# Kernel tuning notes

Measured on AMD Instinct MI355X. Metric: run time of the kernel, lower is better.

Reference implementation:

```python
import jax, jax.numpy as jnp
import numpy as np

N, E = 32, 512          # graphs per batch, padded nodes per graph
IN_DIM = 128            # in_dim
OUT_DIM = 64            # out_dim (d)
N_TYPE = 3              # config.num_edge_type
Q_DIM = 128             # config.input_dim (q_update=False)


def setup_inputs() -> dict:
    key = jax.random.key(0)
    ks = jax.random.split(key, 8)
    s = 0.05  # weight init scale (stands in for xavier_uniform)
    return {
        "input_state": jax.random.normal(ks[0], (N, E, IN_DIM), jnp.float32),
        "adj": jax.random.randint(ks[1], (N, E, E), 0, N_TYPE + 1, jnp.int32),
        "query_vec": jax.random.normal(ks[2], (N, Q_DIM), jnp.float32),
        "node_mask": jax.random.uniform(ks[3], (N, E, 1), jnp.float32),
        "W_type": jax.random.normal(ks[4], (N_TYPE, IN_DIM, OUT_DIM), jnp.float32) * s,
        "a_type": jax.random.normal(ks[5], (N_TYPE, 2 * OUT_DIM, 1), jnp.float32) * s,
        "qattn_W1": jax.random.normal(ks[6], (N_TYPE, Q_DIM, 2 * OUT_DIM), jnp.float32) * s,
        "qattn_W2": jax.random.normal(ks[7], (N_TYPE, 2 * OUT_DIM, 2 * OUT_DIM), jnp.float32) * s,
    }


def reference(input_state, adj, query_vec, node_mask, W_type, a_type, qattn_W1, qattn_W2):
    # Per-type node projections: (T, N, E, d). Dropout omitted (eval mode, p=0).
    h_all = jnp.einsum("nei,tio->tneo", input_state, W_type)

    # Query gate per type: sigmoid(relu(q @ W1) @ W2) -> (T, N, 2d)
    qg = jax.nn.relu(jnp.einsum("nq,tqc->tnc", query_vec, qattn_W1))
    qg = jax.nn.sigmoid(jnp.einsum("tnc,tcd->tnd", qg, qattn_W2))

    d = h_all.shape[-1]
    a_src = a_type[:, :d, 0]   # (T, d) applied to the repeated (source) half
    a_dst = a_type[:, d:, 0]   # (T, d) applied to the tiled (target) half

    # score[t,n,i,j] = lrelu( (h[t,n,i]*qg1[t,n]) . a_src[t] + (h[t,n,j]*qg2[t,n]) . a_dst[t] )
    # This is exactly cat([h_i, h_j]) * q_gate @ a without materializing (N,E,E,2d).
    s_src = jnp.einsum("tned,tnd,td->tne", h_all, qg[..., :d], a_src)
    s_dst = jnp.einsum("tned,tnd,td->tne", h_all, qg[..., d:], a_dst)
    score = jax.nn.leaky_relu(s_src[:, :, :, None] + s_dst[:, :, None, :], 0.2)  # (T,N,E,E)

    # Accumulate scores where adj matches each edge type (1-indexed).
    type_ids = jnp.arange(1, N_TYPE + 1, dtype=adj.dtype)[:, None, None, None]
    scores = jnp.sum(jnp.where(adj[None] == type_ids, score, 0.0), axis=0)  # (N,E,E)

    # Mask non-edges and softmax over dim=2 (target nodes).
    scores = jnp.where(adj > 0, scores, jnp.float32(-1e30))
    coefs = jax.nn.softmax(scores, axis=2)

    # h from the last edge-type loop iteration, node-masked.
    h = h_all[-1] * node_mask  # (N,E,d)

    # out[n,j,:] = sum_i coefs[n,i,j] * h[n,i,:]  (sum over dim=1 in the torch code)
    return jnp.einsum("nij,nid->njd", coefs, h)
```

## Files before the change

kernel.cpp:

```cpp
#include <hip/hip_runtime.h>
#include <hip/hip_bf16.h>

#define N_G 32
#define E_N 512
#define IN_D 128
#define OUT_D 64
#define NT 3
#define Q_D 128

#define WS_WSRC 0
#define WS_WDST 12288
#define WS_SSRC 24576
#define WS_SDST 73728
#define WS_RINV 139264
#define WS_H    155648
#define WS_W2T  679936
#define WS_ADJ2 684032

typedef const float* fp;
typedef __attribute__((ext_vector_type(8))) short short8x;
typedef __attribute__((ext_vector_type(4))) float float4x;

static __device__ inline ushort f2bf(float x) {
  __hip_bfloat16 b = __float2bfloat16(x);
  return *(ushort*)&b;
}
static __device__ inline float bf2f(ushort u) {
  return __uint_as_float((uint)u << 16);
}

__global__ __launch_bounds__(256) void k1_qgate_pack(
    fp qv_g, fp Wt, fp at, fp W1, fp W2,
    const int* __restrict__ adj, float* __restrict__ ws) {
  const int b = blockIdx.x;
  const int t = threadIdx.x;

  if (b >= 96) {
    const int w = t >> 6, lane = t & 63;
    const int R = (b - 96) * 4 + w;
    const int* arow = adj + (size_t)R * E_N;
    uint pack = 0;
    #pragma unroll
    for (int bb = 0; bb < 8; bb++) {
      int a = arow[bb * 64 + lane];
      pack |= (uint)(a & 3) << (2 * bb);
    }
    ((ushort*)(ws + WS_ADJ2))[(size_t)R * 64 + lane] = (ushort)pack;
    return;
  }

  const int tb = b >> 5;
  const int n  = b & 31;
  __shared__ float qv[128];
  __shared__ float ps[8][132];
  __shared__ float g1s[128], g2s[128];
  __shared__ float gsv[64], gdv[64];
  const int h   = t >> 5;
  const int cg_ = (t & 31) << 2;

  if (t < 128) qv[t] = qv_g[n * Q_D + t];
  __syncthreads();

  {
    float a0 = 0.f, a1 = 0.f, a2 = 0.f, a3 = 0.f;
    const float* Wp = W1 + tb * 16384 + (h * 16) * 128 + cg_;
    #pragma unroll
    for (int q = 0; q < 16; q++) {
      float4 wv4 = *(const float4*)(Wp + q * 128);
      float qq = qv[h * 16 + q];
      a0 += qq * wv4.x; a1 += qq * wv4.y; a2 += qq * wv4.z; a3 += qq * wv4.w;
    }
    ps[h][cg_ + 0] = a0; ps[h][cg_ + 1] = a1;
    ps[h][cg_ + 2] = a2; ps[h][cg_ + 3] = a3;
  }
  __syncthreads();
  if (t < 128) {
    float s = 0.f;
    #pragma unroll
    for (int k = 0; k < 8; k++) s += ps[k][t];
    g1s[t] = s > 0.f ? s : 0.f;
  }
  __syncthreads();

  {
    float a0 = 0.f, a1 = 0.f, a2 = 0.f, a3 = 0.f;
    const float* Wp = W2 + tb * 16384 + (h * 16) * 128 + cg_;
    #pragma unroll
    for (int q = 0; q < 16; q++) {
      float4 wv4 = *(const float4*)(Wp + q * 128);
      float qq = g1s[h * 16 + q];
      a0 += qq * wv4.x; a1 += qq * wv4.y; a2 += qq * wv4.z; a3 += qq * wv4.w;
    }
    ps[h][cg_ + 0] = a0; ps[h][cg_ + 1] = a1;
    ps[h][cg_ + 2] = a2; ps[h][cg_ + 3] = a3;
  }
  __syncthreads();
  if (t < 128) {
    float s = 0.f;
    #pragma unroll
    for (int k = 0; k < 8; k++) s += ps[k][t];
    g2s[t] = 1.f / (1.f + __expf(-s));
  }
  __syncthreads();
  if (t < 64) {
    gsv[t] = g2s[t] * at[tb * 128 + t];
    gdv[t] = g2s[64 + t] * at[tb * 128 + 64 + t];
  }
  __syncthreads();

  {
    const int i = t & 127, hf = t >> 7;
    float as = 0.f, ad = 0.f;
    const float* Wp = Wt + tb * 8192 + i * 64 + hf * 32;
    #pragma unroll
    for (int dj = 0; dj < 8; dj++) {
      float4 wv4 = *(const float4*)(Wp + dj * 4);
      const float* gp = gsv + hf * 32 + dj * 4;
      const float* gq = gdv + hf * 32 + dj * 4;
      as += wv4.x * gp[0] + wv4.y * gp[1] + wv4.z * gp[2] + wv4.w * gp[3];
      ad += wv4.x * gq[0] + wv4.y * gq[1] + wv4.z * gq[2] + wv4.w * gq[3];
    }
    ps[hf][i]     = as;
    ps[2 + hf][i] = ad;
  }
  __syncthreads();
  if (t < 128) {
    ws[WS_WSRC + tb * 4096 + n * 128 + t] = ps[0][t] + ps[1][t];
    ws[WS_WDST + tb * 4096 + n * 128 + t] = ps[2][t] + ps[3][t];
  }
  if (tb == 2 && t < 128) {
    int f = n * 256 + t * 2;
    int d = f >> 7, i0 = f & 127;
    uint lo = f2bf(Wt[2 * 8192 + i0 * 64 + d]);
    uint hi = f2bf(Wt[2 * 8192 + (i0 + 1) * 64 + d]);
    ((uint*)(ws + WS_W2T))[f >> 1] = lo | (hi << 16);
  }
}

__global__ __launch_bounds__(256) void k2_h_s(fp X, fp mask,
                                              float* __restrict__ ws) {
  const int n  = blockIdx.x & 31;
  const int e0 = (blockIdx.x >> 5) << 5;
  __shared__ ushort A[32 * 136];
  __shared__ ushort BT[64 * 136];
  __shared__ ushort eT[64 * 40];
  __shared__ float wv[6 * 128];
  const int t = threadIdx.x;
  ushort* hb = (ushort*)(ws + WS_H);
  const ushort* w2t = (const ushort*)(ws + WS_W2T);

  #pragma unroll
  for (int k = 0; k < 4; k++) {
    int f = t + 256 * k;
    int e = f >> 5, iq = f & 31;
    float4 v = *(const float4*)&X[(n * E_N + e0 + e) * IN_D + iq * 4];
    uint2 pk;
    pk.x = (uint)f2bf(v.x) | ((uint)f2bf(v.y) << 16);
    pk.y = (uint)f2bf(v.z) | ((uint)f2bf(v.w) << 16);
    *(uint2*)&A[e * 136 + iq * 4] = pk;
  }
  #pragma unroll
  for (int k = 0; k < 4; k++) {
    int f = t + 256 * k;
    int d = f >> 4, iq8 = f & 15;
    *(uint4*)&BT[d * 136 + iq8 * 8] = *(const uint4*)&w2t[d * 128 + iq8 * 8];
  }
  #pragma unroll
  for (int k = 0; k < 3; k++) {
    int idx = t + 256 * k;
    int row = idx >> 7, i = idx & 127;
    wv[idx] = (row < 3) ? ws[WS_WSRC + row * 4096 + n * 128 + i]
                        : ws[WS_WDST + (row - 3) * 4096 + n * 128 + i];
  }
  __syncthreads();

  const int w = t >> 6, lane = t & 63;
  const int m15 = lane & 15, quad = lane >> 4;
  const int msub = w & 1, dhalf = w >> 1;

  float4x acc2[2];
  acc2[0] = (float4x)(0.f); acc2[1] = (float4x)(0.f);
  #pragma unroll
  for (int ks = 0; ks < 4; ks++) {
    short8x af = *(const short8x*)&A[(msub * 16 + m15) * 136 + ks * 32 + quad * 8];
    #pragma unroll
    for (int dd = 0; dd < 2; dd++) {
      short8x bfv = *(const short8x*)&BT[((dhalf * 2 + dd) * 16 + m15) * 136 + ks * 32 + quad * 8];
      acc2[dd] = __builtin_amdgcn_mfma_f32_16x16x32_bf16(af, bfv, acc2[dd], 0, 0, 0);
    }
  }

  if (t < 192) {
    const int e = t / 6, q = t % 6;
    float acc = 0.f;
    #pragma unroll
    for (int i8 = 0; i8 < 16; i8++) {
      uint4 pk = *(const uint4*)&A[e * 136 + i8 * 8];
      const float* wp = &wv[q * 128 + i8 * 8];
      acc += bf2f((ushort)(pk.x & 0xffff)) * wp[0];
      acc += bf2f((ushort)(pk.x >> 16))    * wp[1];
      acc += bf2f((ushort)(pk.y & 0xffff)) * wp[2];
      acc += bf2f((ushort)(pk.y >> 16))    * wp[3];
      acc += bf2f((ushort)(pk.z & 0xffff)) * wp[4];
      acc += bf2f((ushort)(pk.z >> 16))    * wp[5];
      acc += bf2f((ushort)(pk.w & 0xffff)) * wp[6];
      acc += bf2f((ushort)(pk.w >> 16))    * wp[7];
    }
    if (q < 3) ws[WS_SSRC + q * 16384 + n * 512 + e0 + e] = acc;
    else       ws[WS_SDST + (q - 3) * 16384 + n * 512 + e0 + e] = acc;
  }

  float mv[4];
  #pragma unroll
  for (int rg = 0; rg < 4; rg++)
    mv[rg] = mask[n * E_N + e0 + msub * 16 + quad * 4 + rg];
  #pragma unroll
  for (int dd = 0; dd < 2; dd++) {
    int dRow = (dhalf * 2 + dd) * 16 + m15;
    #pragma unroll
    for (int rg = 0; rg < 4; rg++) {
      int e = msub * 16 + quad * 4 + rg;
      eT[dRow * 40 + e] = f2bf(acc2[dd][rg] * mv[rg]);
    }
  }
  __syncthreads();

  {
    int d = t >> 2, e8 = t & 3;
    *(uint4*)&hb[(n * 64 + d) * 512 + e0 + e8 * 8] =
        *(const uint4*)&eT[d * 40 + e8 * 8];
  }
}

__global__ __launch_bounds__(256) void k3_rows(float* __restrict__ ws) {
  const int n  = blockIdx.x & 31;
  const int rb = (blockIdx.x >> 5) << 5;
  __shared__ float sd[3 * 512];
  const int t = threadIdx.x;
  const ushort* adj2 = (const ushort*)(ws + WS_ADJ2);

  #pragma unroll
  for (int k = 0; k < 6; k++) {
    int idx = t + 256 * k;
    sd[idx] = ws[WS_SDST + (idx >> 9) * 16384 + n * 512 + (idx & 511)];
  }
  __syncthreads();

  const int wave = t >> 6, lane = t & 63;
  #pragma unroll
  for (int rr = 0; rr < 8; rr++) {
    const int i = rb + wave * 8 + rr;
    const float s0 = ws[WS_SSRC + 0 * 16384 + n * 512 + i];
    const float s1 = ws[WS_SSRC + 1 * 16384 + n * 512 + i];
    const float s2 = ws[WS_SSRC + 2 * 16384 + n * 512 + i];
    uint pk = adj2[(size_t)(n * E_N + i) * 64 + lane];

    float sum = 0.f;
    #pragma unroll
    for (int bb = 0; bb < 8; bb++) {
      int a = (pk >> (2 * bb)) & 3;
      if (a > 0) {
        float s = (a == 1) ? s0 : (a == 2 ? s1 : s2);
        float v = s + sd[(a - 1) * 512 + bb * 64 + lane];
        v = v > 0.f ? v : 0.2f * v;
        sum += __expf(v);
      }
    }
    #pragma unroll
    for (int off = 32; off >= 1; off >>= 1) sum += __shfl_xor(sum, off, 64);
    if (lane == 0) ws[WS_RINV + n * 512 + i] = 1.f / sum;
  }
}

__global__ __launch_bounds__(256) void k4_out(float* __restrict__ ws,
                                              float* __restrict__ out) {
  const int n  = blockIdx.x & 31;
  const int j0 = (blockIdx.x >> 5) << 5;
  __shared__ ushort cT[32 * 136];
  __shared__ ushort hT[64 * 136];
  __shared__ ushort aS[128 * 64];
  __shared__ float sdT[3 * 32];
  __shared__ float ssT[3 * 128];
  __shared__ float riT[128];
  const int t = threadIdx.x;
  const ushort* hb = (const ushort*)(ws + WS_H);
  const ushort* adj2 = (const ushort*)(ws + WS_ADJ2);

  if (t < 96) sdT[t] = ws[WS_SDST + (t >> 5) * 16384 + n * 512 + j0 + (t & 31)];

  const int w = t >> 6, lane = t & 63;
  const int m15 = lane & 15, quad = lane >> 4;
  const int msub = w & 1, dhalf = w >> 1;
  const int c   = t & 31;
  const int rpb = t >> 5;
  const int u     = (j0 & 63) + c;
  const int shift = 2 * (j0 >> 6);

  float4x acc[2];
  acc[0] = (float4x)(0.f); acc[1] = (float4x)(0.f);

  for (int it = 0; it < 4; it++) {
    const int i0 = it << 7;

    #pragma unroll
    for (int k = 0; k < 4; k++) {
      int f = t + 256 * k;
      int d = f >> 4, i16 = f & 15;
      *(uint4*)&hT[d * 136 + i16 * 8] =
          *(const uint4*)&hb[(n * 64 + d) * 512 + i0 + i16 * 8];
    }
    #pragma unroll
    for (int k = 0; k < 4; k++) {
      int f = t + 256 * k;
      int r = f >> 3, c8 = f & 7;
      *(uint4*)&aS[r * 64 + c8 * 8] =
          *(const uint4*)&adj2[(size_t)(n * E_N + i0 + r) * 64 + c8 * 8];
    }
    #pragma unroll
    for (int k = 0; k < 2; k++) {
      int idx = t + 256 * k;
      if (idx < 128) riT[idx] = ws[WS_RINV + n * 512 + i0 + idx];
      else {
        int j2 = idx - 128;
        ssT[j2] = ws[WS_SSRC + (j2 >> 7) * 16384 + n * 512 + i0 + (j2 & 127)];
      }
    }
    __syncthreads();

    #pragma unroll
    for (int k = 0; k < 8; k++) {
      int r0 = 2 * (rpb + 8 * k);
      uint pack = 0;
      int a = (aS[r0 * 64 + u] >> shift) & 3;
      if (a > 0) {
        float v = ssT[(a - 1) * 128 + r0] + sdT[(a - 1) * 32 + c];
        v = v > 0.f ? v : 0.2f * v;
        pack = f2bf(__expf(v) * riT[r0]);
      }
      a = (aS[(r0 + 1) * 64 + u] >> shift) & 3;
      if (a > 0) {
        float v = ssT[(a - 1) * 128 + r0 + 1] + sdT[(a - 1) * 32 + c];
        v = v > 0.f ? v : 0.2f * v;
        pack |= (uint)f2bf(__expf(v) * riT[r0 + 1]) << 16;
      }
      *(uint*)&cT[c * 136 + r0] = pack;
    }
    __syncthreads();

    #pragma unroll
    for (int ks = 0; ks < 4; ks++) {
      short8x af = *(const short8x*)&cT[(msub * 16 + m15) * 136 + ks * 32 + quad * 8];
      #pragma unroll
      for (int dd = 0; dd < 2; dd++) {
        short8x bfv = *(const short8x*)&hT[((dhalf * 2 + dd) * 16 + m15) * 136 + ks * 32 + quad * 8];
        acc[dd] = __builtin_amdgcn_mfma_f32_16x16x32_bf16(af, bfv, acc[dd], 0, 0, 0);
      }
    }
    __syncthreads();
  }

  #pragma unroll
  for (int dd = 0; dd < 2; dd++)
    #pragma unroll
    for (int rg = 0; rg < 4; rg++) {
      int j = j0 + msub * 16 + quad * 4 + rg;
      out[(n * E_N + j) * 64 + (dhalf * 2 + dd) * 16 + m15] = acc[dd][rg];
    }
}

extern "C" void kernel_launch(void* const* d_in, const int* in_sizes, int n_in,
                              void* d_out, int out_size, void* d_ws, size_t ws_size,
                              hipStream_t stream) {
  fp input_state  = (fp)d_in[0];
  const int* adj  = (const int*)d_in[1];
  fp query_vec    = (fp)d_in[2];
  fp node_mask    = (fp)d_in[3];
  fp W_type       = (fp)d_in[4];
  fp a_type       = (fp)d_in[5];
  fp qattn_W1     = (fp)d_in[6];
  fp qattn_W2     = (fp)d_in[7];
  float* out = (float*)d_out;
  float* ws  = (float*)d_ws;

  k1_qgate_pack<<<96 + 4096, 256, 0, stream>>>(query_vec, W_type, a_type,
                                               qattn_W1, qattn_W2, adj, ws);
  k2_h_s<<<512, 256, 0, stream>>>(input_state, node_mask, ws);
  k3_rows<<<512, 256, 0, stream>>>(ws);
  k4_out<<<512, 256, 0, stream>>>(ws, out);
}
```

Before: 128.2 us.

## Fuse qgate into projection kernel and adj packing into row-stats kernel

The query-gate computation is merged into the projection/score kernel, so each block recomputes the gated attention vectors for its graph in shared memory instead of writing them to and reading them back from workspace. The adjacency 2-bit packing moves from the first kernel into the row-softmax-denominator kernel, which now reads raw adj once and both packs it and accumulates exp sums. This removes one launch and one full pass over adj. The cost is that each of the 256 blocks repeats the three-type qgate math, and there are half as many blocks for the projection work. Block indexing in the output kernel is also reordered so consecutive blocks share a graph.

```diff
diff --git a/kernel.cpp b/kernel.cpp
--- a/kernel.cpp
+++ b/kernel.cpp
@@ -8,13 +8,10 @@
 #define NT 3
 #define Q_D 128
 
-#define WS_WSRC 0
-#define WS_WDST 12288
 #define WS_SSRC 24576
 #define WS_SDST 73728
 #define WS_RINV 139264
 #define WS_H    155648
-#define WS_W2T  679936
 #define WS_ADJ2 684032
 
 typedef const float* fp;
@@ -29,215 +26,187 @@
   return __uint_as_float((uint)u << 16);
 }
 
-__global__ __launch_bounds__(256) void k1_qgate_pack(
-    fp qv_g, fp Wt, fp at, fp W1, fp W2,
-    const int* __restrict__ adj, float* __restrict__ ws) {
-  const int b = blockIdx.x;
-  const int t = threadIdx.x;
-
-  if (b >= 96) {
-    const int w = t >> 6, lane = t & 63;
-    const int R = (b - 96) * 4 + w;
-    const int* arow = adj + (size_t)R * E_N;
-    uint pack = 0;
-    #pragma unroll
-    for (int bb = 0; bb < 8; bb++) {
-      int a = arow[bb * 64 + lane];
-      pack |= (uint)(a & 3) << (2 * bb);
-    }
-    ((ushort*)(ws + WS_ADJ2))[(size_t)R * 64 + lane] = (ushort)pack;
-    return;
-  }
-
-  const int tb = b >> 5;
-  const int n  = b & 31;
+__global__ __launch_bounds__(256) void kA_qgate_h_s(
+    fp X, fp mask, fp qv_g, fp Wt, fp at, fp W1, fp W2,
+    float* __restrict__ ws) {
+  const int n  = blockIdx.x >> 3;
+  const int eh = blockIdx.x & 7;
   __shared__ float qv[128];
   __shared__ float ps[8][132];
   __shared__ float g1s[128], g2s[128];
   __shared__ float gsv[64], gdv[64];
+  __shared__ float wv[6 * 128];
+  __shared__ ushort BT[64 * 136];
+  __shared__ ushort A[32 * 136];
+  __shared__ ushort eT[64 * 40];
+  const int t = threadIdx.x;
+  ushort* hb = (ushort*)(ws + WS_H);
+
+  #pragma unroll
+  for (int k = 0; k < 8; k++) {
+    int f = k * 1024 + t * 4;
+    int i = f >> 6, d = f & 63;
+    float4 v = *(const float4*)&Wt[2 * 8192 + f];
+    BT[(d + 0) * 136 + i] = f2bf(v.x);
+    BT[(d + 1) * 136 + i] = f2bf(v.y);
+    BT[(d + 2) * 136 + i] = f2bf(v.z);
+    BT[(d + 3) * 136 + i] = f2bf(v.w);
+  }
+  if (t < 128) qv[t] = qv_g[n * Q_D + t];
+  __syncthreads();
+
   const int h   = t >> 5;
   const int cg_ = (t & 31) << 2;
-
-  if (t < 128) qv[t] = qv_g[n * Q_D + t];
-  __syncthreads();
-
-  {
-    float a0 = 0.f, a1 = 0.f, a2 = 0.f, a3 = 0.f;
-    const float* Wp = W1 + tb * 16384 + (h * 16) * 128 + cg_;
-    #pragma unroll
-    for (int q = 0; q < 16; q++) {
-      float4 wv4 = *(const float4*)(Wp + q * 128);
-      float qq = qv[h * 16 + q];
-      a0 += qq * wv4.x; a1 += qq * wv4.y; a2 += qq * wv4.z; a3 += qq * wv4.w;
-    }
-    ps[h][cg_ + 0] = a0; ps[h][cg_ + 1] = a1;
-    ps[h][cg_ + 2] = a2; ps[h][cg_ + 3] = a3;
-  }
-  __syncthreads();
-  if (t < 128) {
-    float s = 0.f;
-    #pragma unroll
-    for (int k = 0; k < 8; k++) s += ps[k][t];
-    g1s[t] = s > 0.f ? s : 0.f;
-  }
-  __syncthreads();
-
-  {
-    float a0 = 0.f, a1 = 0.f, a2 = 0.f, a3 = 0.f;
-    const float* Wp = W2 + tb * 16384 + (h * 16) * 128 + cg_;
-    #pragma unroll
-    for (int q = 0; q < 16; q++) {
-      float4 wv4 = *(const float4*)(Wp + q * 128);
-      float qq = g1s[h * 16 + q];
-      a0 += qq * wv4.x; a1 += qq * wv4.y; a2 += qq * wv4.z; a3 += qq * wv4.w;
-    }
-    ps[h][cg_ + 0] = a0; ps[h][cg_ + 1] = a1;
-    ps[h][cg_ + 2] = a2; ps[h][cg_ + 3] = a3;
-  }
-  __syncthreads();
-  if (t < 128) {
-    float s = 0.f;
-    #pragma unroll
-    for (int k = 0; k < 8; k++) s += ps[k][t];
-    g2s[t] = 1.f / (1.f + __expf(-s));
-  }
-  __syncthreads();
-  if (t < 64) {
-    gsv[t] = g2s[t] * at[tb * 128 + t];
-    gdv[t] = g2s[64 + t] * at[tb * 128 + 64 + t];
-  }
-  __syncthreads();
-
-  {
-    const int i = t & 127, hf = t >> 7;
-    float as = 0.f, ad = 0.f;
-    const float* Wp = Wt + tb * 8192 + i * 64 + hf * 32;
-    #pragma unroll
-    for (int dj = 0; dj < 8; dj++) {
-      float4 wv4 = *(const float4*)(Wp + dj * 4);
-      const float* gp = gsv + hf * 32 + dj * 4;
-      const float* gq = gdv + hf * 32 + dj * 4;
-      as += wv4.x * gp[0] + wv4.y * gp[1] + wv4.z * gp[2] + wv4.w * gp[3];
-      ad += wv4.x * gq[0] + wv4.y * gq[1] + wv4.z * gq[2] + wv4.w * gq[3];
-    }
-    ps[hf][i]     = as;
-    ps[2 + hf][i] = ad;
-  }
-  __syncthreads();
-  if (t < 128) {
-    ws[WS_WSRC + tb * 4096 + n * 128 + t] = ps[0][t] + ps[1][t];
-    ws[WS_WDST + tb * 4096 + n * 128 + t] = ps[2][t] + ps[3][t];
-  }
-  if (tb == 2 && t < 128) {
-    int f = n * 256 + t * 2;
-    int d = f >> 7, i0 = f & 127;
-    uint lo = f2bf(Wt[2 * 8192 + i0 * 64 + d]);
-    uint hi = f2bf(Wt[2 * 8192 + (i0 + 1) * 64 + d]);
-    ((uint*)(ws + WS_W2T))[f >> 1] = lo | (hi << 16);
-  }
-}
-
-__global__ __launch_bounds__(256) void k2_h_s(fp X, fp mask,
-                                              float* __restrict__ ws) {
-  const int n  = blockIdx.x & 31;
-  const int e0 = (blockIdx.x >> 5) << 5;
-  __shared__ ushort A[32 * 136];
-  __shared__ ushort BT[64 * 136];
-  __shared__ ushort eT[64 * 40];
-  __shared__ float wv[6 * 128];
-  const int t = threadIdx.x;
-  ushort* hb = (ushort*)(ws + WS_H);
-  const ushort* w2t = (const ushort*)(ws + WS_W2T);
-
-  #pragma unroll
-  for (int k = 0; k < 4; k++) {
-    int f = t + 256 * k;
-    int e = f >> 5, iq = f & 31;
-    float4 v = *(const float4*)&X[(n * E_N + e0 + e) * IN_D + iq * 4];
-    uint2 pk;
-    pk.x = (uint)f2bf(v.x) | ((uint)f2bf(v.y) << 16);
-    pk.y = (uint)f2bf(v.z) | ((uint)f2bf(v.w) << 16);
-    *(uint2*)&A[e * 136 + iq * 4] = pk;
-  }
-  #pragma unroll
-  for (int k = 0; k < 4; k++) {
-    int f = t + 256 * k;
-    int d = f >> 4, iq8 = f & 15;
-    *(uint4*)&BT[d * 136 + iq8 * 8] = *(const uint4*)&w2t[d * 128 + iq8 * 8];
-  }
-  #pragma unroll
-  for (int k = 0; k < 3; k++) {
-    int idx = t + 256 * k;
-    int row = idx >> 7, i = idx & 127;
-    wv[idx] = (row < 3) ? ws[WS_WSRC + row * 4096 + n * 128 + i]
-                        : ws[WS_WDST + (row - 3) * 4096 + n * 128 + i];
-  }
-  __syncthreads();
+  for (int tt = 0; tt < 3; tt++) {
+    {
+      float a0 = 0.f, a1 = 0.f, a2 = 0.f, a3 = 0.f;
+      const float* Wp = W1 + tt * 16384 + (h * 16) * 128 + cg_;
+      #pragma unroll
+      for (int q = 0; q < 16; q++) {
+        float4 wv4 = *(const float4*)(Wp + q * 128);
+        float qq = qv[h * 16 + q];
+        a0 += qq * wv4.x; a1 += qq * wv4.y; a2 += qq * wv4.z; a3 += qq * wv4.w;
+      }
+      ps[h][cg_ + 0] = a0; ps[h][cg_ + 1] = a1;
+      ps[h][cg_ + 2] = a2; ps[h][cg_ + 3] = a3;
+    }
+    __syncthreads();
+    if (t < 128) {
+      float s = 0.f;
+      #pragma unroll
+      for (int k = 0; k < 8; k++) s += ps[k][t];
+      g1s[t] = s > 0.f ? s : 0.f;
+    }
+    __syncthreads();
+    {
+      float a0 = 0.f, a1 = 0.f, a2 = 0.f, a3 = 0.f;
+      const float* Wp = W2 + tt * 16384 + (h * 16) * 128 + cg_;
+      #pragma unroll
+      for (int q = 0; q < 16; q++) {
+        float4 wv4 = *(const float4*)(Wp + q * 128);
+        float qq = g1s[h * 16 + q];
+        a0 += qq * wv4.x; a1 += qq * wv4.y; a2 += qq * wv4.z; a3 += qq * wv4.w;
+      }
+      ps[h][cg_ + 0] = a0; ps[h][cg_ + 1] = a1;
+      ps[h][cg_ + 2] = a2; ps[h][cg_ + 3] = a3;
+    }
+    __syncthreads();
+    if (t < 128) {
+      float s = 0.f;
+      #pragma unroll
+      for (int k = 0; k < 8; k++) s += ps[k][t];
+      g2s[t] = 1.f / (1.f + __expf(-s));
+    }
+    __syncthreads();
+    if (t < 64) {
+      gsv[t] = g2s[t] * at[tt * 128 + t];
+      gdv[t] = g2s[64 + t] * at[tt * 128 + 64 + t];
+    }
+    __syncthreads();
+    {
+      const int i = t & 127, hf = t >> 7;
+      float as = 0.f, ad = 0.f;
+      const float* Wp = Wt + tt * 8192 + i * 64 + hf * 32;
+      #pragma unroll
+      for (int dj = 0; dj < 8; dj++) {
+        float4 wv4 = *(const float4*)(Wp + dj * 4);
+        const float* gp = gsv + hf * 32 + dj * 4;
+        const float* gq = gdv + hf * 32 + dj * 4;
+        as += wv4.x * gp[0] + wv4.y * gp[1] + wv4.z * gp[2] + wv4.w * gp[3];
+        ad += wv4.x * gq[0] + wv4.y * gq[1] + wv4.z * gq[2] + wv4.w * gq[3];
+      }
+      ps[hf][i]     = as;
+      ps[2 + hf][i] = ad;
+    }
+    __syncthreads();
+    if (t < 128) {
+      wv[tt * 128 + t]       = ps[0][t] + ps[1][t];
+      wv[(3 + tt) * 128 + t] = ps[2][t] + ps[3][t];
+    }
+    __syncthreads();
+  }
 
   const int w = t >> 6, lane = t & 63;
   const int m15 = lane & 15, quad = lane >> 4;
   const int msub = w & 1, dhalf = w >> 1;
 
-  float4x acc2[2];
-  acc2[0] = (float4x)(0.f); acc2[1] = (float4x)(0.f);
-  #pragma unroll
-  for (int ks = 0; ks < 4; ks++) {
-    short8x af = *(const short8x*)&A[(msub * 16 + m15) * 136 + ks * 32 + quad * 8];
+  for (int sub = 0; sub < 2; sub++) {
+    const int e0 = eh * 64 + sub * 32;
+
+    #pragma unroll
+    for (int k = 0; k < 4; k++) {
+      int f = t + 256 * k;
+      int e = f >> 5, iq = f & 31;
+      float4 v = *(const float4*)&X[(n * E_N + e0 + e) * IN_D + iq * 4];
+      uint2 pk;
+      pk.x = (uint)f2bf(v.x) | ((uint)f2bf(v.y) << 16);
+      pk.y = (uint)f2bf(v.z) | ((uint)f2bf(v.w) << 16);
+      *(uint2*)&A[e * 136 + iq * 4] = pk;
+    }
+    __syncthreads();
+
+    float4x acc2[2];
+    acc2[0] = (float4x)(0.f); acc2[1] = (float4x)(0.f);
+    #pragma unroll
+    for (int ks = 0; ks < 4; ks++) {
+      short8x af = *(const short8x*)&A[(msub * 16 + m15) * 136 + ks * 32 + quad * 8];
+      #pragma unroll
+      for (int dd = 0; dd < 2; dd++) {
+        short8x bfv = *(const short8x*)&BT[((dhalf * 2 + dd) * 16 + m15) * 136 + ks * 32 + quad * 8];
+        acc2[dd] = __builtin_amdgcn_mfma_f32_16x16x32_bf16(af, bfv, acc2[dd], 0, 0, 0);
+      }
+    }
+
+    if (t < 192) {
+      const int e = t / 6, q = t % 6;
+      float acc = 0.f;
+      #pragma unroll
+      for (int i8 = 0; i8 < 16; i8++) {
+        uint4 pk = *(const uint4*)&A[e * 136 + i8 * 8];
+        const float* wp = &wv[q * 128 + i8 * 8];
+        acc += bf2f((ushort)(pk.x & 0xffff)) * wp[0];
+        acc += bf2f((ushort)(pk.x >> 16))    * wp[1];
+        acc += bf2f((ushort)(pk.y & 0xffff)) * wp[2];
+        acc += bf2f((ushort)(pk.y >> 16))    * wp[3];
+        acc += bf2f((ushort)(pk.z & 0xffff)) * wp[4];
+        acc += bf2f((ushort)(pk.z >> 16))    * wp[5];
+        acc += bf2f((ushort)(pk.w & 0xffff)) * wp[6];
+        acc += bf2f((ushort)(pk.w >> 16))    * wp[7];
+      }
+      if (q < 3) ws[WS_SSRC + q * 16384 + n * 512 + e0 + e] = acc;
+      else       ws[WS_SDST + (q - 3) * 16384 + n * 512 + e0 + e] = acc;
+    }
+
+    float mv[4];
+    #pragma unroll
+    for (int rg = 0; rg < 4; rg++)
+      mv[rg] = mask[n * E_N + e0 + msub * 16 + quad * 4 + rg];
     #pragma unroll
     for (int dd = 0; dd < 2; dd++) {
-      short8x bfv = *(const short8x*)&BT[((dhalf * 2 + dd) * 16 + m15) * 136 + ks * 32 + quad * 8];
-      acc2[dd] = __builtin_amdgcn_mfma_f32_16x16x32_bf16(af, bfv, acc2[dd], 0, 0, 0);
-    }
-  }
-
-  if (t < 192) {
-    const int e = t / 6, q = t % 6;
-    float acc = 0.f;
-    #pragma unroll
-    for (int i8 = 0; i8 < 16; i8++) {
-      uint4 pk = *(const uint4*)&A[e * 136 + i8 * 8];
-      const float* wp = &wv[q * 128 + i8 * 8];
-      acc += bf2f((ushort)(pk.x & 0xffff)) * wp[0];
-      acc += bf2f((ushort)(pk.x >> 16))    * wp[1];
-      acc += bf2f((ushort)(pk.y & 0xffff)) * wp[2];
-      acc += bf2f((ushort)(pk.y >> 16))    * wp[3];
-      acc += bf2f((ushort)(pk.z & 0xffff)) * wp[4];
-      acc += bf2f((ushort)(pk.z >> 16))    * wp[5];
-      acc += bf2f((ushort)(pk.w & 0xffff)) * wp[6];
-      acc += bf2f((ushort)(pk.w >> 16))    * wp[7];
-    }
-    if (q < 3) ws[WS_SSRC + q * 16384 + n * 512 + e0 + e] = acc;
-    else       ws[WS_SDST + (q - 3) * 16384 + n * 512 + e0 + e] = acc;
-  }
-
-  float mv[4];
-  #pragma unroll
-  for (int rg = 0; rg < 4; rg++)
-    mv[rg] = mask[n * E_N + e0 + msub * 16 + quad * 4 + rg];
-  #pragma unroll
-  for (int dd = 0; dd < 2; dd++) {
-    int dRow = (dhalf * 2 + dd) * 16 + m15;
-    #pragma unroll
-    for (int rg = 0; rg < 4; rg++) {
-      int e = msub * 16 + quad * 4 + rg;
-      eT[dRow * 40 + e] = f2bf(acc2[dd][rg] * mv[rg]);
-    }
-  }
-  __syncthreads();
-
-  {
-    int d = t >> 2, e8 = t & 3;
-    *(uint4*)&hb[(n * 64 + d) * 512 + e0 + e8 * 8] =
-        *(const uint4*)&eT[d * 40 + e8 * 8];
-  }
-}
-
-__global__ __launch_bounds__(256) void k3_rows(float* __restrict__ ws) {
-  const int n  = blockIdx.x & 31;
-  const int rb = (blockIdx.x >> 5) << 5;
+      int dRow = (dhalf * 2 + dd) * 16 + m15;
+      #pragma unroll
+      for (int rg = 0; rg < 4; rg++) {
+        int e = msub * 16 + quad * 4 + rg;
+        eT[dRow * 40 + e] = f2bf(acc2[dd][rg] * mv[rg]);
+      }
+    }
+    __syncthreads();
+
+    {
+      int d = t >> 2, e8 = t & 3;
+      *(uint4*)&hb[(n * 64 + d) * 512 + e0 + e8 * 8] =
+          *(const uint4*)&eT[d * 40 + e8 * 8];
+    }
+  }
+}
+
+__global__ __launch_bounds__(256) void kB_rowstats(const int* __restrict__ adj,
+                                                   float* __restrict__ ws) {
+  const int n  = blockIdx.x >> 7;
+  const int ib = blockIdx.x & 127;
   __shared__ float sd[3 * 512];
   const int t = threadIdx.x;
-  const ushort* adj2 = (const ushort*)(ws + WS_ADJ2);
+  ushort* adj2 = (ushort*)(ws + WS_ADJ2);
 
   #pragma unroll
   for (int k = 0; k < 6; k++) {
@@ -247,35 +216,36 @@
   __syncthreads();
 
   const int wave = t >> 6, lane = t & 63;
-  #pragma unroll
-  for (int rr = 0; rr < 8; rr++) {
-    const int i = rb + wave * 8 + rr;
-    const float s0 = ws[WS_SSRC + 0 * 16384 + n * 512 + i];
-    const float s1 = ws[WS_SSRC + 1 * 16384 + n * 512 + i];
-    const float s2 = ws[WS_SSRC + 2 * 16384 + n * 512 + i];
-    uint pk = adj2[(size_t)(n * E_N + i) * 64 + lane];
-
-    float sum = 0.f;
-    #pragma unroll
-    for (int bb = 0; bb < 8; bb++) {
-      int a = (pk >> (2 * bb)) & 3;
-      if (a > 0) {
-        float s = (a == 1) ? s0 : (a == 2 ? s1 : s2);
-        float v = s + sd[(a - 1) * 512 + bb * 64 + lane];
-        v = v > 0.f ? v : 0.2f * v;
-        sum += __expf(v);
-      }
-    }
-    #pragma unroll
-    for (int off = 32; off >= 1; off >>= 1) sum += __shfl_xor(sum, off, 64);
-    if (lane == 0) ws[WS_RINV + n * 512 + i] = 1.f / sum;
-  }
-}
-
-__global__ __launch_bounds__(256) void k4_out(float* __restrict__ ws,
+  const int i = ib * 4 + wave;
+  const float s0 = ws[WS_SSRC + 0 * 16384 + n * 512 + i];
+  const float s1 = ws[WS_SSRC + 1 * 16384 + n * 512 + i];
+  const float s2 = ws[WS_SSRC + 2 * 16384 + n * 512 + i];
+  const int* arow = &adj[(n * E_N + i) * E_N];
+
+  float sum = 0.f;
+  uint pack = 0;
+  #pragma unroll
+  for (int b = 0; b < 8; b++) {
+    int j = b * 64 + lane;
+    int a = arow[j];
+    pack |= (uint)(a & 3) << (2 * b);
+    if (a > 0) {
+      float s = (a == 1) ? s0 : (a == 2 ? s1 : s2);
+      float v = s + sd[(a - 1) * 512 + j];
+      v = v > 0.f ? v : 0.2f * v;
+      sum += __expf(v);
+    }
+  }
+  #pragma unroll
+  for (int off = 32; off >= 1; off >>= 1) sum += __shfl_xor(sum, off, 64);
+  if (lane == 0) ws[WS_RINV + n * 512 + i] = 1.f / sum;
+  adj2[(n * E_N + i) * 64 + lane] = (ushort)pack;
+}
+
+__global__ __launch_bounds__(256) void kC_out(float* __restrict__ ws,
                                               float* __restrict__ out) {
-  const int n  = blockIdx.x & 31;
-  const int j0 = (blockIdx.x >> 5) << 5;
+  const int n  = blockIdx.x >> 4;
+  const int j0 = (blockIdx.x & 15) << 5;
   __shared__ ushort cT[32 * 136];
   __shared__ ushort hT[64 * 136];
   __shared__ ushort aS[128 * 64];
@@ -382,9 +352,8 @@
   float* out = (float*)d_out;
   float* ws  = (float*)d_ws;
 
-  k1_qgate_pack<<<96 + 4096, 256, 0, stream>>>(query_vec, W_type, a_type,
-                                               qattn_W1, qattn_W2, adj, ws);
-  k2_h_s<<<512, 256, 0, stream>>>(input_state, node_mask, ws);
-  k3_rows<<<512, 256, 0, stream>>>(ws);
-  k4_out<<<512, 256, 0, stream>>>(ws, out);
-}
+  kA_qgate_h_s<<<256, 256, 0, stream>>>(input_state, node_mask, query_vec,
+                                        W_type, a_type, qattn_W1, qattn_W2, ws);
+  kB_rowstats<<<32 * 128, 256, 0, stream>>>(adj, ws);
+  kC_out<<<32 * 16, 256, 0, stream>>>(ws, out);
+}
```

Result: no change. 128.3 us (+0.1%).
